# Kernel optimization log

Hardware: AMD Instinct MI355X
Metric: run time of the kernel (lower is better)

## Reference

```python
import jax, jax.numpy as jnp
import numpy as np

H = 32        # query heads
KV = 8        # kv heads
HD = 128      # head_dim
EPS = 1e-6
THETA = 1e6
T = 2048
D = 4096


def _rms_norm(x, w):
    # x: [T, heads, HD]
    var = jnp.mean(jnp.square(x), axis=-1, keepdims=True)
    return x * jax.lax.rsqrt(var + EPS) * w


def _rope(x, cos, sin):
    # NEOX-style rotary: split last dim in halves. x: [T, heads, HD]
    x1, x2 = jnp.split(x, 2, axis=-1)
    return jnp.concatenate([x1 * cos - x2 * sin, x2 * cos + x1 * sin], axis=-1)


def setup_inputs() -> dict:
    key = jax.random.key(0)
    k1, k2, k3 = jax.random.split(key, 3)
    s = 1.0 / np.sqrt(D)
    return {
        "positions": jnp.arange(T, dtype=jnp.int32),
        "hidden_states": jax.random.normal(k1, (T, D), dtype=jnp.float32),
        "w_qkv": jax.random.normal(k2, (D, (H + 2 * KV) * HD), dtype=jnp.float32) * s,
        "q_norm_w": jnp.ones((HD,), dtype=jnp.float32),
        "k_norm_w": jnp.ones((HD,), dtype=jnp.float32),
        "w_o": jax.random.normal(k3, (H * HD, D), dtype=jnp.float32) * s,
    }


def reference(positions, hidden_states, w_qkv, q_norm_w, k_norm_w, w_o):
    scale = HD ** -0.5
    qkv = hidden_states @ w_qkv                              # [T, (H+2KV)*HD]
    q = qkv[:, : H * HD].reshape(T, H, HD)
    k = qkv[:, H * HD : (H + KV) * HD].reshape(T, KV, HD)
    v = qkv[:, (H + KV) * HD :].reshape(T, KV, HD)

    # per-head RMSNorm on q/k (Qwen3 QK-norm)
    q = _rms_norm(q, q_norm_w)
    k = _rms_norm(k, k_norm_w)

    # RoPE
    inv_freq = 1.0 / (THETA ** (jnp.arange(0, HD, 2, dtype=jnp.float32) / HD))
    freqs = positions.astype(jnp.float32)[:, None] * inv_freq  # [T, HD/2]
    cos = jnp.cos(freqs)[:, None, :]                            # [T, 1, HD/2]
    sin = jnp.sin(freqs)[:, None, :]
    q = _rope(q, cos, sin)
    k = _rope(k, cos, sin)

    # GQA: repeat kv heads
    rep = H // KV
    k = jnp.repeat(k, rep, axis=1)                           # [T, H, HD]
    v = jnp.repeat(v, rep, axis=1)

    # causal SDPA
    scores = jnp.einsum("thd,shd->hts", q, k) * scale        # [H, T, T]
    causal = jnp.tril(jnp.ones((T, T), dtype=bool))
    scores = jnp.where(causal[None], scores, jnp.finfo(scores.dtype).min)
    probs = jax.nn.softmax(scores, axis=-1)
    attn = jnp.einsum("hts,shd->thd", probs, v).reshape(T, H * HD)

    return attn @ w_o                                        # [T, D]
```

## Files before the change

kernel.cpp:

```cpp
#include <hip/hip_runtime.h>

#define TT   2048
#define DD   4096
#define NH   32
#define NKVH 8
#define HDM  128
#define KD   4096
#define NQKV 6144

typedef unsigned short u16;
typedef short v8s __attribute__((ext_vector_type(8)));
typedef float v4f __attribute__((ext_vector_type(4)));

#define QSCALE 0.12751744547734565f
#define EOFF   17.312340490667562f

__device__ __forceinline__ u16 f2bf(float f) {
    unsigned u = __builtin_bit_cast(unsigned, f);
    u += 0x7fffu + ((u >> 16) & 1u);
    return (u16)(u >> 16);
}
__device__ __forceinline__ float bf2f(u16 h) {
    return __builtin_bit_cast(float, ((unsigned)h) << 16);
}
__device__ __forceinline__ void gl2lds16(const void* g, void* l) {
    using gv = const __attribute__((address_space(1))) void;
    using lv = __attribute__((address_space(3))) void;
    __builtin_amdgcn_global_load_lds((gv*)g, (lv*)l, 16, 0, 0);
}

__device__ __forceinline__ void transpose_tile64(const float* __restrict__ in,
                                                 u16* __restrict__ out,
                                                 int K, int N, int n0, int k0,
                                                 float* tile, int t) {
    int rc = t >> 4, cc = (t & 15) * 4;
#pragma unroll
    for (int p = 0; p < 4; ++p) {
        int k = p * 16 + rc;
        float4 v = *(const float4*)&in[(size_t)(k0 + k) * N + n0 + cc];
        tile[k * 65 + cc] = v.x; tile[k * 65 + cc + 1] = v.y;
        tile[k * 65 + cc + 2] = v.z; tile[k * 65 + cc + 3] = v.w;
    }
    __syncthreads();
    int rn = t >> 3, ck = (t & 7) * 8;
#pragma unroll
    for (int p = 0; p < 2; ++p) {
        int n = p * 32 + rn;
        v8s tv;
#pragma unroll
        for (int j = 0; j < 8; ++j) tv[j] = (short)f2bf(tile[(ck + j) * 65 + n]);
        *(v8s*)&out[(size_t)(n0 + n) * K + k0 + ck] = tv;
    }
}

__global__ __launch_bounds__(256) void prep_all_kernel(const float* __restrict__ hidden,
                                                       u16* __restrict__ hid_bf,
                                                       const int* __restrict__ positions,
                                                       float* __restrict__ cosT,
                                                       float* __restrict__ sinT,
                                                       const float* __restrict__ w_qkv,
                                                       u16* __restrict__ wqkv_t) {
    __shared__ float tile[64 * 65];
    int b = blockIdx.x;
    if (b < 4096) {
        size_t i = ((size_t)b * 256 + threadIdx.x) * 8;
        float4 a = *(const float4*)&hidden[i];
        float4 c = *(const float4*)&hidden[i + 4];
        v8s tv;
        tv[0] = (short)f2bf(a.x); tv[1] = (short)f2bf(a.y);
        tv[2] = (short)f2bf(a.z); tv[3] = (short)f2bf(a.w);
        tv[4] = (short)f2bf(c.x); tv[5] = (short)f2bf(c.y);
        tv[6] = (short)f2bf(c.z); tv[7] = (short)f2bf(c.w);
        *(v8s*)&hid_bf[i] = tv;
    } else if (b < 4608) {
        int idx = (b - 4096) * 256 + threadIdx.x;
        int tp = idx >> 6, i = idx & 63;
        float invf = exp2f(-(float)i * 0.31143075889569023f);
        float f = (float)positions[tp] * invf;
        cosT[idx] = cosf(f);
        sinT[idx] = sinf(f);
    } else {
        int bx = b - 4608;
        int n0 = (bx % 96) * 64, k0 = (bx / 96) * 64;
        transpose_tile64(w_qkv, wqkv_t, 4096, NQKV, n0, k0, tile, threadIdx.x);
    }
}

template <int MODE>
__global__ __launch_bounds__(256) void gemm_bt_kernel(
    const u16* __restrict__ A, const u16* __restrict__ Bt, float* __restrict__ C, int N,
    const float* __restrict__ qw, const float* __restrict__ kw,
    const float* __restrict__ cosT, const float* __restrict__ sinT,
    u16* __restrict__ Qb, u16* __restrict__ Kb, u16* __restrict__ Vt)
{
    __shared__ __align__(16) u16 smem[16896];
    u16* As = smem;
    u16* Bs = smem + 8192;
    int tid = threadIdx.x;
    int wave = tid >> 6, lane = tid & 63;
    int quad = lane >> 4, l15 = lane & 15;
    int lm = l15 & 7;
    int wm = wave >> 1, wn = wave & 1;
    int m0 = blockIdx.y * 128, n0 = blockIdx.x * 128;

    v4f acc[4][4];
    v4f z4 = {0.f, 0.f, 0.f, 0.f};
#pragma unroll
    for (int mi = 0; mi < 4; ++mi)
#pragma unroll
        for (int ni = 0; ni < 4; ++ni) acc[mi][ni] = z4;

    int rsub = lane >> 3;
    int cg = (lane & 7) ^ rsub;
    const u16* Ag = &A[(size_t)m0 * KD + cg * 8];
    const u16* Bg = &Bt[(size_t)n0 * KD + cg * 8];

    for (int k0 = 0; k0 < KD; k0 += 64) {
        __syncthreads();
#pragma unroll
        for (int c = 0; c < 4; ++c) {
            int ch = wave * 4 + c;
            int row = ch * 8 + rsub;
            gl2lds16(&Ag[(size_t)row * KD + k0], &As[ch * 512]);
            gl2lds16(&Bg[(size_t)row * KD + k0], &Bs[ch * 512]);
        }
        __syncthreads();
#pragma unroll
        for (int ks = 0; ks < 2; ++ks) {
            v8s af[4], bfr[4];
#pragma unroll
            for (int mi = 0; mi < 4; ++mi) {
                int ar = wm * 64 + mi * 16 + l15;
                af[mi] = *(const v8s*)&As[ar * 64 + ((((ks << 2) + quad) ^ lm) << 3)];
            }
#pragma unroll
            for (int ni = 0; ni < 4; ++ni) {
                int br = wn * 64 + ni * 16 + l15;
                bfr[ni] = *(const v8s*)&Bs[br * 64 + ((((ks << 2) + quad) ^ lm) << 3)];
            }
#pragma unroll
            for (int mi = 0; mi < 4; ++mi)
#pragma unroll
                for (int ni = 0; ni < 4; ++ni)
                    acc[mi][ni] = __builtin_amdgcn_mfma_f32_16x16x32_bf16(
                        af[mi], bfr[ni], acc[mi][ni], 0, 0, 0);
        }
    }

    if (MODE == 0) {
#pragma unroll
        for (int mi = 0; mi < 4; ++mi)
#pragma unroll
            for (int ni = 0; ni < 4; ++ni)
#pragma unroll
                for (int r = 0; r < 4; ++r)
                    C[(size_t)(m0 + wm * 64 + mi * 16 + quad * 4 + r) * N +
                      (n0 + wn * 64 + ni * 16 + l15)] = acc[mi][ni][r];
    } else {
        __syncthreads();
        u16* Ct = smem;
#pragma unroll
        for (int mi = 0; mi < 4; ++mi)
#pragma unroll
            for (int ni = 0; ni < 4; ++ni)
#pragma unroll
                for (int r = 0; r < 4; ++r)
                    Ct[(wm * 64 + mi * 16 + quad * 4 + r) * 132 + wn * 64 + ni * 16 + l15] =
                        f2bf(acc[mi][ni][r]);
        __syncthreads();
        int head = blockIdx.x;
        int t0 = blockIdx.y * 128;
        if (head < 40) {
            if (tid < 128) {
                int row = tid;
                const float* w = (head < 32) ? qw : kw;
                float ss = 0.f;
                for (int i = 0; i < 128; ++i) {
                    float x = bf2f(Ct[row * 132 + i]);
                    ss += x * x;
                }
                float rs = rsqrtf(ss * (1.0f / 128.0f) + 1e-6f);
                if (head < 32) rs *= QSCALE;
                int ti = t0 + row;
                for (int i = 0; i < 64; ++i) {
                    float x1 = bf2f(Ct[row * 132 + i]) * rs * w[i];
                    float x2 = bf2f(Ct[row * 132 + 64 + i]) * rs * w[64 + i];
                    float c = cosT[ti * 64 + i], s = sinT[ti * 64 + i];
                    Ct[row * 132 + i]      = f2bf(x1 * c - x2 * s);
                    Ct[row * 132 + 64 + i] = f2bf(x2 * c + x1 * s);
                }
            }
            __syncthreads();
            u16* dst = (head < 32) ? &Qb[((size_t)head * TT + t0) * HDM]
                                   : &Kb[((size_t)(head - 32) * TT + t0) * HDM];
            for (int cix = tid; cix < 128 * 16; cix += 256) {
                int row = cix >> 4, part = (cix & 15) * 8;
                v8s tv;
#pragma unroll
                for (int j = 0; j < 8; ++j) tv[j] = (short)Ct[row * 132 + part + j];
                *(v8s*)&dst[row * HDM + part] = tv;
            }
        } else {
            int kvh = head - 40;
            if (tid < 128) {
                int hd = tid;
#pragma unroll
                for (int tb = 0; tb < 16; ++tb) {
                    v8s tv;
#pragma unroll
                    for (int j = 0; j < 8; ++j) tv[j] = (short)Ct[(tb * 8 + j) * 132 + hd];
                    *(v8s*)&Vt[((size_t)kvh * HDM + hd) * TT + t0 + tb * 8] = tv;
                }
            }
        }
    }
}

__global__ __launch_bounds__(256) void attn_plus_kernel(
    const u16* __restrict__ Qb, const u16* __restrict__ Kb,
    const u16* __restrict__ Vt, u16* __restrict__ Ob,
    const float* __restrict__ w_o, u16* __restrict__ wo_t)
{
    __shared__ __align__(16) char smem_raw[40960];
    int tid = threadIdx.x;
    if (blockIdx.x >= 1024) {
        int bx = blockIdx.x - 1024;
        int n0 = (bx & 63) * 64, k0 = (bx >> 6) * 64;
        transpose_tile64(w_o, wo_t, 4096, 4096, n0, k0, (float*)smem_raw, tid);
        return;
    }
    u16* Kl = (u16*)smem_raw;
    u16* Vl = (u16*)(smem_raw + 16384);
    u16* Pl = (u16*)(smem_raw + 32768);
    int wave = tid >> 6, lane = tid & 63;
    int quad = lane >> 4, l15 = lane & 15;
    int idx = blockIdx.x;
    int h = idx & 31;
    int qb = 31 - (idx >> 5);
    int kv = h >> 2;
    int q0 = qb * 64;
    int lm = l15 & 7;

    v8s qf[4];
    {
        const u16* qr = &Qb[((size_t)h * TT + q0 + wave * 16 + l15) * HDM];
#pragma unroll
        for (int ks = 0; ks < 4; ++ks) qf[ks] = *(const v8s*)&qr[ks * 32 + quad * 8];
    }

    v4f z4 = {0.f, 0.f, 0.f, 0.f};
    v4f of[8];
#pragma unroll
    for (int i = 0; i < 8; ++i) of[i] = z4;
    float lsum[4];
#pragma unroll
    for (int r = 0; r < 4; ++r) lsum[r] = 0.f;
    u16* Pw = &Pl[wave * 1024];

    for (int s0 = 0; s0 <= q0; s0 += 64) {
        __syncthreads();
#pragma unroll
        for (int c = 0; c < 4; ++c) {
            int ch = wave * 4 + c;
            int rk = ch * 4 + (lane >> 4);
            int ck = (lane & 15) ^ (rk & 7);
            gl2lds16(&Kb[((size_t)kv * TT + s0 + rk) * HDM + ck * 8], &Kl[ch * 512]);
            int rv = ch * 8 + (lane >> 3);
            int cv = (lane & 7) ^ (rv & 7);
            gl2lds16(&Vt[((size_t)kv * HDM + rv) * TT + s0 + cv * 8], &Vl[ch * 512]);
        }
        __syncthreads();
        v4f sf[4];
#pragma unroll
        for (int nt = 0; nt < 4; ++nt) {
            v4f cacc = z4;
#pragma unroll
            for (int ks = 0; ks < 4; ++ks)
                cacc = __builtin_amdgcn_mfma_f32_16x16x32_bf16(
                    qf[ks],
                    *(const v8s*)&Kl[(nt * 16 + l15) * 128 + (((ks * 4 + quad) ^ lm) << 3)],
                    cacc, 0, 0, 0);
            sf[nt] = cacc;
        }
        if (s0 == q0) {
#pragma unroll
            for (int nt = 0; nt < 4; ++nt) {
                int sg = s0 + nt * 16 + l15;
#pragma unroll
                for (int r = 0; r < 4; ++r) {
                    int qg = q0 + wave * 16 + quad * 4 + r;
                    if (sg > qg) sf[nt][r] = -3.0e38f;
                }
            }
        }
#pragma unroll
        for (int nt = 0; nt < 4; ++nt)
#pragma unroll
            for (int r = 0; r < 4; ++r) {
                float p = exp2f(sf[nt][r] - EOFF);
                sf[nt][r] = p;
                lsum[r] += p;
            }
#pragma unroll
        for (int nt = 0; nt < 4; ++nt)
#pragma unroll
            for (int r = 0; r < 4; ++r) {
                int row = quad * 4 + r;
                int pch = ((nt << 1) + (l15 >> 3)) ^ (row & 7);
                Pw[row * 64 + pch * 8 + (l15 & 7)] = f2bf(sf[nt][r]);
            }
#pragma unroll
        for (int sub = 0; sub < 2; ++sub) {
            v8s pa = *(const v8s*)&Pw[l15 * 64 + ((((sub << 2) + quad) ^ lm) << 3)];
#pragma unroll
            for (int nt = 0; nt < 8; ++nt)
                of[nt] = __builtin_amdgcn_mfma_f32_16x16x32_bf16(
                    pa,
                    *(const v8s*)&Vl[(nt * 16 + l15) * 64 + ((((sub << 2) + quad) ^ lm) << 3)],
                    of[nt], 0, 0, 0);
        }
    }
#pragma unroll
    for (int off = 1; off < 16; off <<= 1)
#pragma unroll
        for (int r = 0; r < 4; ++r) lsum[r] += __shfl_xor(lsum[r], off, 64);
    float invl[4];
#pragma unroll
    for (int r = 0; r < 4; ++r) invl[r] = 1.0f / lsum[r];
#pragma unroll
    for (int nt = 0; nt < 8; ++nt)
#pragma unroll
        for (int r = 0; r < 4; ++r)
            Ob[(size_t)(q0 + wave * 16 + quad * 4 + r) * (NH * HDM) + h * HDM + nt * 16 + l15] =
                f2bf(of[nt][r] * invl[r]);
}

extern "C" void kernel_launch(void* const* d_in, const int* in_sizes, int n_in,
                              void* d_out, int out_size, void* d_ws, size_t ws_size,
                              hipStream_t stream)
{
    (void)in_sizes; (void)n_in; (void)out_size; (void)ws_size;
    const int*   positions = (const int*)d_in[0];
    const float* hidden    = (const float*)d_in[1];
    const float* w_qkv     = (const float*)d_in[2];
    const float* q_norm_w  = (const float*)d_in[3];
    const float* k_norm_w  = (const float*)d_in[4];
    const float* w_o       = (const float*)d_in[5];
    float* out = (float*)d_out;
    char* ws = (char*)d_ws;
    char* ob = (char*)d_out;

    u16* hid_bf = (u16*)(ws + 0);
    u16* attnO  = (u16*)(ws + 0);
    u16* wqkv_t = (u16*)(ws + (size_t)16777216);
    u16* wo_t   = (u16*)(ws + (size_t)16777216);

    u16*   Qb   = (u16*)(ob + 0);
    u16*   Kb   = (u16*)(ob + (size_t)16777216);
    u16*   Vt   = (u16*)(ob + (size_t)20971520);
    float* cosT = (float*)(ob + (size_t)25165824);
    float* sinT = (float*)(ob + (size_t)25690112);

    prep_all_kernel<<<10752, 256, 0, stream>>>(hidden, hid_bf, positions, cosT, sinT,
                                               w_qkv, wqkv_t);

    gemm_bt_kernel<1><<<dim3(48, 16), 256, 0, stream>>>(
        hid_bf, wqkv_t, nullptr, NQKV, q_norm_w, k_norm_w, cosT, sinT, Qb, Kb, Vt);

    attn_plus_kernel<<<5120, 256, 0, stream>>>(Qb, Kb, Vt, attnO, w_o, wo_t);

    gemm_bt_kernel<0><<<dim3(32, 16), 256, 0, stream>>>(
        attnO, wo_t, out, 4096, nullptr, nullptr, nullptr, nullptr, nullptr, nullptr, nullptr);
}
```

Before: 487.1 us.

## Enlarge attention query tile to 128 rows and split O-projection GEMM tile

The attention kernel now processes 128 query rows per block, with each wave handling two 16-row subtiles. Each K/V tile loaded into LDS is therefore reused across twice as many queries, and the block count is halved. Waves whose rows lie entirely before the current key tile skip compute but still join the shared loads, which introduces some idle work along the diagonal. The output-projection GEMM becomes a dedicated kernel with 128x64 tiles, doubling its block count to 1024 so more blocks are in flight, at the cost of less reuse per block.

```diff
diff --git a/kernel.cpp b/kernel.cpp
--- a/kernel.cpp
+++ b/kernel.cpp
@@ -86,9 +86,8 @@
     }
 }
 
-template <int MODE>
-__global__ __launch_bounds__(256) void gemm_bt_kernel(
-    const u16* __restrict__ A, const u16* __restrict__ Bt, float* __restrict__ C, int N,
+__global__ __launch_bounds__(256) void gemm_qkv_kernel(
+    const u16* __restrict__ A, const u16* __restrict__ Bt,
     const float* __restrict__ qw, const float* __restrict__ kw,
     const float* __restrict__ cosT, const float* __restrict__ sinT,
     u16* __restrict__ Qb, u16* __restrict__ Kb, u16* __restrict__ Vt)
@@ -147,73 +146,131 @@
         }
     }
 
-    if (MODE == 0) {
-#pragma unroll
-        for (int mi = 0; mi < 4; ++mi)
-#pragma unroll
-            for (int ni = 0; ni < 4; ++ni)
-#pragma unroll
-                for (int r = 0; r < 4; ++r)
-                    C[(size_t)(m0 + wm * 64 + mi * 16 + quad * 4 + r) * N +
-                      (n0 + wn * 64 + ni * 16 + l15)] = acc[mi][ni][r];
+    __syncthreads();
+    u16* Ct = smem;
+#pragma unroll
+    for (int mi = 0; mi < 4; ++mi)
+#pragma unroll
+        for (int ni = 0; ni < 4; ++ni)
+#pragma unroll
+            for (int r = 0; r < 4; ++r)
+                Ct[(wm * 64 + mi * 16 + quad * 4 + r) * 132 + wn * 64 + ni * 16 + l15] =
+                    f2bf(acc[mi][ni][r]);
+    __syncthreads();
+    int head = blockIdx.x;
+    int t0 = blockIdx.y * 128;
+    if (head < 40) {
+        if (tid < 128) {
+            int row = tid;
+            const float* w = (head < 32) ? qw : kw;
+            float ss = 0.f;
+            for (int i = 0; i < 128; ++i) {
+                float x = bf2f(Ct[row * 132 + i]);
+                ss += x * x;
+            }
+            float rs = rsqrtf(ss * (1.0f / 128.0f) + 1e-6f);
+            if (head < 32) rs *= QSCALE;
+            int ti = t0 + row;
+            for (int i = 0; i < 64; ++i) {
+                float x1 = bf2f(Ct[row * 132 + i]) * rs * w[i];
+                float x2 = bf2f(Ct[row * 132 + 64 + i]) * rs * w[64 + i];
+                float c = cosT[ti * 64 + i], s = sinT[ti * 64 + i];
+                Ct[row * 132 + i]      = f2bf(x1 * c - x2 * s);
+                Ct[row * 132 + 64 + i] = f2bf(x2 * c + x1 * s);
+            }
+        }
+        __syncthreads();
+        u16* dst = (head < 32) ? &Qb[((size_t)head * TT + t0) * HDM]
+                               : &Kb[((size_t)(head - 32) * TT + t0) * HDM];
+        for (int cix = tid; cix < 128 * 16; cix += 256) {
+            int row = cix >> 4, part = (cix & 15) * 8;
+            v8s tv;
+#pragma unroll
+            for (int j = 0; j < 8; ++j) tv[j] = (short)Ct[row * 132 + part + j];
+            *(v8s*)&dst[row * HDM + part] = tv;
+        }
     } else {
-        __syncthreads();
-        u16* Ct = smem;
-#pragma unroll
-        for (int mi = 0; mi < 4; ++mi)
-#pragma unroll
-            for (int ni = 0; ni < 4; ++ni)
-#pragma unroll
-                for (int r = 0; r < 4; ++r)
-                    Ct[(wm * 64 + mi * 16 + quad * 4 + r) * 132 + wn * 64 + ni * 16 + l15] =
-                        f2bf(acc[mi][ni][r]);
-        __syncthreads();
-        int head = blockIdx.x;
-        int t0 = blockIdx.y * 128;
-        if (head < 40) {
-            if (tid < 128) {
-                int row = tid;
-                const float* w = (head < 32) ? qw : kw;
-                float ss = 0.f;
-                for (int i = 0; i < 128; ++i) {
-                    float x = bf2f(Ct[row * 132 + i]);
-                    ss += x * x;
-                }
-                float rs = rsqrtf(ss * (1.0f / 128.0f) + 1e-6f);
-                if (head < 32) rs *= QSCALE;
-                int ti = t0 + row;
-                for (int i = 0; i < 64; ++i) {
-                    float x1 = bf2f(Ct[row * 132 + i]) * rs * w[i];
-                    float x2 = bf2f(Ct[row * 132 + 64 + i]) * rs * w[64 + i];
-                    float c = cosT[ti * 64 + i], s = sinT[ti * 64 + i];
-                    Ct[row * 132 + i]      = f2bf(x1 * c - x2 * s);
-                    Ct[row * 132 + 64 + i] = f2bf(x2 * c + x1 * s);
-                }
-            }
-            __syncthreads();
-            u16* dst = (head < 32) ? &Qb[((size_t)head * TT + t0) * HDM]
-                                   : &Kb[((size_t)(head - 32) * TT + t0) * HDM];
-            for (int cix = tid; cix < 128 * 16; cix += 256) {
-                int row = cix >> 4, part = (cix & 15) * 8;
+        int kvh = head - 40;
+        if (tid < 128) {
+            int hd = tid;
+#pragma unroll
+            for (int tb = 0; tb < 16; ++tb) {
                 v8s tv;
 #pragma unroll
-                for (int j = 0; j < 8; ++j) tv[j] = (short)Ct[row * 132 + part + j];
-                *(v8s*)&dst[row * HDM + part] = tv;
-            }
-        } else {
-            int kvh = head - 40;
-            if (tid < 128) {
-                int hd = tid;
-#pragma unroll
-                for (int tb = 0; tb < 16; ++tb) {
-                    v8s tv;
-#pragma unroll
-                    for (int j = 0; j < 8; ++j) tv[j] = (short)Ct[(tb * 8 + j) * 132 + hd];
-                    *(v8s*)&Vt[((size_t)kvh * HDM + hd) * TT + t0 + tb * 8] = tv;
-                }
-            }
-        }
-    }
+                for (int j = 0; j < 8; ++j) tv[j] = (short)Ct[(tb * 8 + j) * 132 + hd];
+                *(v8s*)&Vt[((size_t)kvh * HDM + hd) * TT + t0 + tb * 8] = tv;
+            }
+        }
+    }
+}
+
+__global__ __launch_bounds__(256) void gemm_o_kernel(
+    const u16* __restrict__ A, const u16* __restrict__ Bt, float* __restrict__ C)
+{
+    __shared__ __align__(16) u16 smem[12288];
+    u16* As = smem;
+    u16* Bs = smem + 8192;
+    int tid = threadIdx.x;
+    int wave = tid >> 6, lane = tid & 63;
+    int quad = lane >> 4, l15 = lane & 15;
+    int lm = l15 & 7;
+    int wm = wave >> 1, wn = wave & 1;
+    int m0 = blockIdx.y * 128, n0 = blockIdx.x * 64;
+
+    v4f acc[4][2];
+    v4f z4 = {0.f, 0.f, 0.f, 0.f};
+#pragma unroll
+    for (int mi = 0; mi < 4; ++mi)
+#pragma unroll
+        for (int ni = 0; ni < 2; ++ni) acc[mi][ni] = z4;
+
+    int rsub = lane >> 3;
+    int cg = (lane & 7) ^ rsub;
+    const u16* Ag = &A[(size_t)m0 * KD + cg * 8];
+    const u16* Bg = &Bt[(size_t)n0 * KD + cg * 8];
+
+    for (int k0 = 0; k0 < KD; k0 += 64) {
+        __syncthreads();
+#pragma unroll
+        for (int c = 0; c < 4; ++c) {
+            int ch = wave * 4 + c;
+            gl2lds16(&Ag[(size_t)(ch * 8 + rsub) * KD + k0], &As[ch * 512]);
+        }
+#pragma unroll
+        for (int c = 0; c < 2; ++c) {
+            int ch = wave * 2 + c;
+            gl2lds16(&Bg[(size_t)(ch * 8 + rsub) * KD + k0], &Bs[ch * 512]);
+        }
+        __syncthreads();
+#pragma unroll
+        for (int ks = 0; ks < 2; ++ks) {
+            v8s af[4], bfr[2];
+#pragma unroll
+            for (int mi = 0; mi < 4; ++mi) {
+                int ar = wm * 64 + mi * 16 + l15;
+                af[mi] = *(const v8s*)&As[ar * 64 + ((((ks << 2) + quad) ^ lm) << 3)];
+            }
+#pragma unroll
+            for (int ni = 0; ni < 2; ++ni) {
+                int br = wn * 32 + ni * 16 + l15;
+                bfr[ni] = *(const v8s*)&Bs[br * 64 + ((((ks << 2) + quad) ^ lm) << 3)];
+            }
+#pragma unroll
+            for (int mi = 0; mi < 4; ++mi)
+#pragma unroll
+                for (int ni = 0; ni < 2; ++ni)
+                    acc[mi][ni] = __builtin_amdgcn_mfma_f32_16x16x32_bf16(
+                        af[mi], bfr[ni], acc[mi][ni], 0, 0, 0);
+        }
+    }
+#pragma unroll
+    for (int mi = 0; mi < 4; ++mi)
+#pragma unroll
+        for (int ni = 0; ni < 2; ++ni)
+#pragma unroll
+            for (int r = 0; r < 4; ++r)
+                C[(size_t)(m0 + wm * 64 + mi * 16 + quad * 4 + r) * DD +
+                  (n0 + wn * 32 + ni * 16 + l15)] = acc[mi][ni][r];
 }
 
 __global__ __launch_bounds__(256) void attn_plus_kernel(
@@ -221,10 +278,10 @@
     const u16* __restrict__ Vt, u16* __restrict__ Ob,
     const float* __restrict__ w_o, u16* __restrict__ wo_t)
 {
-    __shared__ __align__(16) char smem_raw[40960];
+    __shared__ __align__(16) char smem_raw[49152];
     int tid = threadIdx.x;
-    if (blockIdx.x >= 1024) {
-        int bx = blockIdx.x - 1024;
+    if (blockIdx.x >= 512) {
+        int bx = blockIdx.x - 512;
         int n0 = (bx & 63) * 64, k0 = (bx >> 6) * 64;
         transpose_tile64(w_o, wo_t, 4096, 4096, n0, k0, (float*)smem_raw, tid);
         return;
@@ -236,28 +293,34 @@
     int quad = lane >> 4, l15 = lane & 15;
     int idx = blockIdx.x;
     int h = idx & 31;
-    int qb = 31 - (idx >> 5);
+    int qb = 15 - (idx >> 5);
     int kv = h >> 2;
-    int q0 = qb * 64;
+    int q0 = qb * 128;
+    int rbase = q0 + wave * 32;
     int lm = l15 & 7;
 
-    v8s qf[4];
-    {
-        const u16* qr = &Qb[((size_t)h * TT + q0 + wave * 16 + l15) * HDM];
-#pragma unroll
-        for (int ks = 0; ks < 4; ++ks) qf[ks] = *(const v8s*)&qr[ks * 32 + quad * 8];
+    v8s qf[2][4];
+#pragma unroll
+    for (int m = 0; m < 2; ++m) {
+        const u16* qr = &Qb[((size_t)h * TT + rbase + m * 16 + l15) * HDM];
+#pragma unroll
+        for (int ks = 0; ks < 4; ++ks) qf[m][ks] = *(const v8s*)&qr[ks * 32 + quad * 8];
     }
 
     v4f z4 = {0.f, 0.f, 0.f, 0.f};
-    v4f of[8];
-#pragma unroll
-    for (int i = 0; i < 8; ++i) of[i] = z4;
-    float lsum[4];
-#pragma unroll
-    for (int r = 0; r < 4; ++r) lsum[r] = 0.f;
-    u16* Pw = &Pl[wave * 1024];
-
-    for (int s0 = 0; s0 <= q0; s0 += 64) {
+    v4f of[2][8];
+#pragma unroll
+    for (int m = 0; m < 2; ++m)
+#pragma unroll
+        for (int i = 0; i < 8; ++i) of[m][i] = z4;
+    float lsum[2][4];
+#pragma unroll
+    for (int m = 0; m < 2; ++m)
+#pragma unroll
+        for (int r = 0; r < 4; ++r) lsum[m][r] = 0.f;
+    u16* Pw = &Pl[wave * 2048];
+
+    for (int s0 = 0; s0 <= q0 + 64; s0 += 64) {
         __syncthreads();
 #pragma unroll
         for (int c = 0; c < 4; ++c) {
@@ -270,69 +333,77 @@
             gl2lds16(&Vt[((size_t)kv * HDM + rv) * TT + s0 + cv * 8], &Vl[ch * 512]);
         }
         __syncthreads();
-        v4f sf[4];
+        if (s0 > rbase + 31) continue;
+        bool diag = (s0 + 63 > rbase);
+        v4f sf[2][4];
 #pragma unroll
         for (int nt = 0; nt < 4; ++nt) {
-            v4f cacc = z4;
-#pragma unroll
-            for (int ks = 0; ks < 4; ++ks)
-                cacc = __builtin_amdgcn_mfma_f32_16x16x32_bf16(
-                    qf[ks],
-                    *(const v8s*)&Kl[(nt * 16 + l15) * 128 + (((ks * 4 + quad) ^ lm) << 3)],
-                    cacc, 0, 0, 0);
-            sf[nt] = cacc;
-        }
-        if (s0 == q0) {
-#pragma unroll
-            for (int nt = 0; nt < 4; ++nt) {
-                int sg = s0 + nt * 16 + l15;
+            v4f c0 = z4, c1 = z4;
+#pragma unroll
+            for (int ks = 0; ks < 4; ++ks) {
+                v8s kf = *(const v8s*)&Kl[(nt * 16 + l15) * 128 + (((ks * 4 + quad) ^ lm) << 3)];
+                c0 = __builtin_amdgcn_mfma_f32_16x16x32_bf16(qf[0][ks], kf, c0, 0, 0, 0);
+                c1 = __builtin_amdgcn_mfma_f32_16x16x32_bf16(qf[1][ks], kf, c1, 0, 0, 0);
+            }
+            sf[0][nt] = c0;
+            sf[1][nt] = c1;
+        }
+        if (diag) {
+#pragma unroll
+            for (int m = 0; m < 2; ++m)
+#pragma unroll
+                for (int nt = 0; nt < 4; ++nt) {
+                    int sg = s0 + nt * 16 + l15;
+#pragma unroll
+                    for (int r = 0; r < 4; ++r) {
+                        int qg = rbase + m * 16 + quad * 4 + r;
+                        if (sg > qg) sf[m][nt][r] = -3.0e38f;
+                    }
+                }
+        }
+#pragma unroll
+        for (int m = 0; m < 2; ++m)
+#pragma unroll
+            for (int nt = 0; nt < 4; ++nt)
 #pragma unroll
                 for (int r = 0; r < 4; ++r) {
-                    int qg = q0 + wave * 16 + quad * 4 + r;
-                    if (sg > qg) sf[nt][r] = -3.0e38f;
+                    float p = exp2f(sf[m][nt][r] - EOFF);
+                    lsum[m][r] += p;
+                    int row = m * 16 + quad * 4 + r;
+                    int pch = ((nt << 1) + (l15 >> 3)) ^ (row & 7);
+                    Pw[row * 64 + pch * 8 + (l15 & 7)] = f2bf(p);
                 }
-            }
-        }
-#pragma unroll
-        for (int nt = 0; nt < 4; ++nt)
-#pragma unroll
-            for (int r = 0; r < 4; ++r) {
-                float p = exp2f(sf[nt][r] - EOFF);
-                sf[nt][r] = p;
-                lsum[r] += p;
-            }
-#pragma unroll
-        for (int nt = 0; nt < 4; ++nt)
-#pragma unroll
-            for (int r = 0; r < 4; ++r) {
-                int row = quad * 4 + r;
-                int pch = ((nt << 1) + (l15 >> 3)) ^ (row & 7);
-                Pw[row * 64 + pch * 8 + (l15 & 7)] = f2bf(sf[nt][r]);
-            }
 #pragma unroll
         for (int sub = 0; sub < 2; ++sub) {
-            v8s pa = *(const v8s*)&Pw[l15 * 64 + ((((sub << 2) + quad) ^ lm) << 3)];
-#pragma unroll
-            for (int nt = 0; nt < 8; ++nt)
-                of[nt] = __builtin_amdgcn_mfma_f32_16x16x32_bf16(
-                    pa,
-                    *(const v8s*)&Vl[(nt * 16 + l15) * 64 + ((((sub << 2) + quad) ^ lm) << 3)],
-                    of[nt], 0, 0, 0);
+            int swz = (((sub << 2) + quad) ^ lm) << 3;
+            v8s pa0 = *(const v8s*)&Pw[l15 * 64 + swz];
+            v8s pa1 = *(const v8s*)&Pw[(16 + l15) * 64 + swz];
+#pragma unroll
+            for (int nt = 0; nt < 8; ++nt) {
+                v8s vf = *(const v8s*)&Vl[(nt * 16 + l15) * 64 + swz];
+                of[0][nt] = __builtin_amdgcn_mfma_f32_16x16x32_bf16(pa0, vf, of[0][nt], 0, 0, 0);
+                of[1][nt] = __builtin_amdgcn_mfma_f32_16x16x32_bf16(pa1, vf, of[1][nt], 0, 0, 0);
+            }
         }
     }
 #pragma unroll
     for (int off = 1; off < 16; off <<= 1)
 #pragma unroll
-        for (int r = 0; r < 4; ++r) lsum[r] += __shfl_xor(lsum[r], off, 64);
-    float invl[4];
-#pragma unroll
-    for (int r = 0; r < 4; ++r) invl[r] = 1.0f / lsum[r];
-#pragma unroll
-    for (int nt = 0; nt < 8; ++nt)
-#pragma unroll
-        for (int r = 0; r < 4; ++r)
-            Ob[(size_t)(q0 + wave * 16 + quad * 4 + r) * (NH * HDM) + h * HDM + nt * 16 + l15] =
-                f2bf(of[nt][r] * invl[r]);
+        for (int m = 0; m < 2; ++m)
+#pragma unroll
+            for (int r = 0; r < 4; ++r) lsum[m][r] += __shfl_xor(lsum[m][r], off, 64);
+#pragma unroll
+    for (int m = 0; m < 2; ++m) {
+        float invl[4];
+#pragma unroll
+        for (int r = 0; r < 4; ++r) invl[r] = 1.0f / lsum[m][r];
+#pragma unroll
+        for (int nt = 0; nt < 8; ++nt)
+#pragma unroll
+            for (int r = 0; r < 4; ++r)
+                Ob[(size_t)(rbase + m * 16 + quad * 4 + r) * (NH * HDM) + h * HDM + nt * 16 + l15] =
+                    f2bf(of[m][nt][r] * invl[r]);
+    }
 }
 
 extern "C" void kernel_launch(void* const* d_in, const int* in_sizes, int n_in,
@@ -364,11 +435,10 @@
     prep_all_kernel<<<10752, 256, 0, stream>>>(hidden, hid_bf, positions, cosT, sinT,
                                                w_qkv, wqkv_t);
 
-    gemm_bt_kernel<1><<<dim3(48, 16), 256, 0, stream>>>(
-        hid_bf, wqkv_t, nullptr, NQKV, q_norm_w, k_norm_w, cosT, sinT, Qb, Kb, Vt);
-
-    attn_plus_kernel<<<5120, 256, 0, stream>>>(Qb, Kb, Vt, attnO, w_o, wo_t);
-
-    gemm_bt_kernel<0><<<dim3(32, 16), 256, 0, stream>>>(
-        attnO, wo_t, out, 4096, nullptr, nullptr, nullptr, nullptr, nullptr, nullptr, nullptr);
-}
+    gemm_qkv_kernel<<<dim3(48, 16), 256, 0, stream>>>(
+        hid_bf, wqkv_t, q_norm_w, k_norm_w, cosT, sinT, Qb, Kb, Vt);
+
+    attn_plus_kernel<<<4608, 256, 0, stream>>>(Qb, Kb, Vt, attnO, w_o, wo_t);
+
+    gemm_o_kernel<<<dim3(64, 16), 256, 0, stream>>>(attnO, wo_t, out);
+}
```

Result: slower. 504.0 us (+3.5%).
